# Kernel tuning notes

Measured on AMD Instinct MI355X. Metric: run time of the kernel, lower is better.

Reference implementation:

```python
import jax, jax.numpy as jnp
import numpy as np

B, S, D_IN = 64, 3072, 128
E, H, OUT = 64, 256, 10
K, STRIDE = 3, 3
T_OUT = (S - K) // STRIDE + 1  # 1024


def setup_inputs() -> dict:
    key = jax.random.key(0)
    ks = jax.random.split(key, 8)
    inputs = jax.random.normal(ks[0], (B, S, D_IN), dtype=jnp.float32)
    r = jnp.zeros((B, E, T_OUT), dtype=jnp.float32)
    s = 0.05
    conv_w = jax.random.normal(ks[1], (E, D_IN, K), dtype=jnp.float32) * s
    conv_b = jax.random.normal(ks[2], (E,), dtype=jnp.float32) * s
    w_ih = jax.random.normal(ks[3], (4 * H, E), dtype=jnp.float32) * s
    w_hh = jax.random.normal(ks[4], (4 * H, H), dtype=jnp.float32) * s
    b_ih = jax.random.normal(ks[5], (4 * H,), dtype=jnp.float32) * s
    b_hh = jax.random.normal(ks[6], (4 * H,), dtype=jnp.float32) * s
    lin_w = jax.random.normal(ks[7], (OUT, H), dtype=jnp.float32) * s
    lin_b = jnp.zeros((OUT,), dtype=jnp.float32)
    return {"inputs": inputs, "r": r, "batch_size": B,
            "conv_w": conv_w, "conv_b": conv_b,
            "w_ih": w_ih, "w_hh": w_hh, "b_ih": b_ih, "b_hh": b_hh,
            "lin_w": lin_w, "lin_b": lin_b}


def _forward(inputs, conv_w, conv_b, w_ih, w_hh, b_ih, b_hh, lin_w, lin_b):
    # F.normalize(inputs, dim=2): L2-normalize feature dim (eps=1e-12)
    norm = jnp.linalg.norm(inputs, axis=2, keepdims=True)
    x = inputs / jnp.maximum(norm, 1e-12)
    # permute(0,2,1): [B, D_IN, S], then Conv1d stride 3
    x = jnp.transpose(x, (0, 2, 1))
    emb = jax.lax.conv_general_dilated(
        x, conv_w, window_strides=(STRIDE,), padding='VALID',
        dimension_numbers=('NCH', 'OIH', 'NCH'))
    emb = emb + conv_b[None, :, None]
    act = jax.nn.relu(emb)                      # [B, E, T_OUT]
    xs = jnp.transpose(act, (2, 0, 1))          # [T, B, E] for scan

    def step(carry, x_t):
        h, c = carry
        gates = x_t @ w_ih.T + b_ih + h @ w_hh.T + b_hh  # [B, 4H]
        i_g, f_g, g_g, o_g = jnp.split(gates, 4, axis=1)
        c_new = jax.nn.sigmoid(f_g) * c + jax.nn.sigmoid(i_g) * jnp.tanh(g_g)
        h_new = jax.nn.sigmoid(o_g) * jnp.tanh(c_new)
        return (h_new, c_new), None

    h0 = jnp.zeros((inputs.shape[0], H), dtype=inputs.dtype)
    c0 = jnp.zeros((inputs.shape[0], H), dtype=inputs.dtype)
    (h_last, _), _ = jax.lax.scan(step, (h0, c0), xs)
    return h_last @ lin_w.T + lin_b             # [B, OUT]


def reference(inputs, r, batch_size, conv_w, conv_b, w_ih, w_hh, b_ih, b_hh, lin_w, lin_b):
    # mode='plain': r and batch_size are unused by the math
    return _forward(inputs, conv_w, conv_b, w_ih, w_hh, b_ih, b_hh, lin_w, lin_b)
```

## Files before the change

kernel.cpp:

```cpp
#include <hip/hip_runtime.h>
#include <math.h>

#define B_   64
#define S_   3072
#define DIN  128
#define E_   64
#define H_   256
#define OUT_ 10
#define T_   1024
#define NG   32
#define GB   2
#define NCH  8
#define NLINES 192
#define SLOT 168

#define ACT_BYTES   (B_*E_*T_*4)
#define HBUF_OFF    ACT_BYTES
#define HBUF_BYTES  (NG*2*NLINES*16)
#define HFINAL_OFF  (HBUF_OFF + HBUF_BYTES)
#define HFINAL_BYTES (NG*GB*H_*4)

typedef float f32x4 __attribute__((ext_vector_type(4)));

__device__ __forceinline__ f32x4 coh_load_f32x4(const float* p) {
  f32x4 r;
  asm volatile("global_load_dwordx4 %0, %1, off sc0 sc1\n\ts_waitcnt vmcnt(0)"
               : "=v"(r) : "v"(p) : "memory");
  return r;
}
__device__ __forceinline__ void coh_store_f32x4(float* p, f32x4 v) {
  asm volatile("global_store_dwordx4 %0, %1, off sc0 sc1" :: "v"(p), "v"(v) : "memory");
}

__device__ __forceinline__ float fast_sigmoid(float x) {
  return __builtin_amdgcn_rcpf(1.0f + __expf(-x));
}
__device__ __forceinline__ float fast_tanh(float x) {
  return 2.0f * __builtin_amdgcn_rcpf(1.0f + __expf(-2.0f * x)) - 1.0f;
}

__global__ __launch_bounds__(512, 1) void conv_kernel(
    const float* __restrict__ in,
    const float* __restrict__ cw,
    const float* __restrict__ cb,
    float* __restrict__ actT)
{
  extern __shared__ float xs[];
  float4* xs4 = (float4*)xs;
  const int bid = blockIdx.x;
  const int b  = bid >> 4;
  const int tb = bid & 15;
  const int tid = threadIdx.x;

  const float4* gin = (const float4*)(in + (size_t)b*S_*DIN + (size_t)tb*192*DIN);
  #pragma unroll
  for (int i = 0; i < 12; ++i) {
    int f4 = tid + i*512;
    int r = f4 >> 5, dq = f4 & 31;
    xs4[r*32 + (dq ^ (r & 7))] = gin[f4];
  }
  __syncthreads();

  const int wv = tid >> 6, ln = tid & 63;
  for (int rr = 0; rr < 24; ++rr) {
    int r = wv*24 + rr;
    int u = r*32 + ((ln >> 1) ^ (r & 7));
    float2* p = (float2*)((char*)xs + (size_t)u*16 + (size_t)(ln & 1)*8);
    float2 v = *p;
    float s = v.x*v.x + v.y*v.y;
    #pragma unroll
    for (int off = 32; off >= 1; off >>= 1) s += __shfl_xor(s, off);
    float inv = 1.0f / fmaxf(sqrtf(s), 1e-12f);
    v.x *= inv; v.y *= inv;
    *p = v;
  }
  __syncthreads();

  const int eo = __builtin_amdgcn_readfirstlane(wv);
  float acc[8];
  #pragma unroll
  for (int j = 0; j < 8; ++j) acc[j] = cb[eo*8 + j];

  const int r0 = 3*ln, r1 = 3*ln + 1, r2 = 3*ln + 2;
  #pragma unroll 4
  for (int dq = 0; dq < 32; ++dq) {
    float4 x0 = xs4[r0*32 + (dq ^ (r0 & 7))];
    float4 x1 = xs4[r1*32 + (dq ^ (r1 & 7))];
    float4 x2 = xs4[r2*32 + (dq ^ (r2 & 7))];
    #pragma unroll
    for (int j = 0; j < 8; ++j) {
      const float* wp = cw + (size_t)(eo*8 + j)*(DIN*3) + dq*12;
      acc[j] += x0.x*wp[0] + x1.x*wp[1] + x2.x*wp[2]
              + x0.y*wp[3] + x1.y*wp[4] + x2.y*wp[5]
              + x0.z*wp[6] + x1.z*wp[7] + x2.z*wp[8]
              + x0.w*wp[9] + x1.w*wp[10] + x2.w*wp[11];
    }
  }

  const int tg = tb*64 + ln;
  #pragma unroll
  for (int j = 0; j < 8; ++j) {
    int e = eo*8 + j;
    actT[(size_t)b*E_*T_ + (size_t)e*T_ + tg] = fmaxf(acc[j], 0.0f);
  }
}

__device__ __forceinline__ void kmap(int hidx, int& kh, int& slot) {
  kh = (hidx < 160) ? 0 : 1;
  slot = (hidx < 160) ? hidx : hidx - 160;
}

__global__ __launch_bounds__(512, 1) void lstm_kernel(
    const float* __restrict__ actT,
    const float* __restrict__ w_ih,
    const float* __restrict__ w_hh,
    const float* __restrict__ b_ih,
    const float* __restrict__ b_hh,
    float* hbuf,
    float* hfinal)
{
  __shared__ float sl[2][2][2][SLOT];

  const int bid = blockIdx.x;
  const int g = bid & 31;
  const int q = bid >> 5;
  const int tid = threadIdx.x;
  const int w = tid >> 6;
  const int l = tid & 63;

  const int khalf = l & 1;
  const int m     = (l >> 1) & 3;
  const int o     = l >> 3;
  const int b     = w & 1;
  const int wh    = w >> 1;
  const int hh    = wh*8 + o;
  const int row   = m*256 + 32*q + hh;

  float4 wv[40];
  if (khalf == 0) {
    const float4* ph = (const float4*)(w_hh + (size_t)row*H_);
    #pragma unroll
    for (int i = 0; i < 40; ++i) wv[i] = ph[i];
  } else {
    const float4* ph = (const float4*)(w_hh + (size_t)row*H_) + 40;
    #pragma unroll
    for (int i = 0; i < 24; ++i) wv[i] = ph[i];
    const float4* px = (const float4*)(w_ih + (size_t)row*E_);
    #pragma unroll
    for (int i = 0; i < 16; ++i) wv[24+i] = px[i];
  }
  const float bias = (khalf == 0) ? (b_ih[row] + b_hh[row]) : 0.0f;

  for (int i = tid; i < 2*2*2*SLOT; i += 512) ((float*)sl)[i] = 0.0f;

  const int pq = tid / 24, pw = (tid % 24) / 3, ps = tid % 3;
  const bool is_poll = (tid < 192) && (pq != q);
  const int pb = pw & 1;
  const int phh0 = 32*pq + (pw >> 1)*8 + 3*ps;
  const int pcnt = (ps == 2) ? 2 : 3;

  const bool is_x = (tid >= 384);
  const int xi = tid - 384, xb = (xi >> 6) & 1, xe = xi & 63;
  const float* actp = actT + (size_t)((g*GB + xb)*E_ + xe)*T_;

  const int ss = l / 24;
  const bool is_store = ((l % 24) == 0);
  const int sline = q*24 + w*3 + ss;
  const int shh0 = wh*8 + 3*ss;
  const int scnt = (ss == 2) ? 2 : 3;

  float* hb = hbuf + (size_t)g*(2*NLINES*4);

  __syncthreads();

  float c = 0.0f;
  for (int t = 0; t < T_; ++t) {
    const int p = t & 1;

    float xval = 0.0f;
    if (is_x) xval = actp[t];

    if (t > 0 && is_poll) {
      const float* lp = hb + (size_t)(p*NLINES + tid)*4;
      f32x4 v = coh_load_f32x4(lp);
      while (__float_as_int(v[3]) != t) v = coh_load_f32x4(lp);
      #pragma unroll
      for (int j = 0; j < 3; ++j) {
        if (j < pcnt) {
          int kh, slot; kmap(phh0 + j, kh, slot);
          sl[p][pb][kh][slot] = v[j];
        }
      }
    }
    if (is_x) sl[p][xb][1][96 + xe] = xval;
    __syncthreads();

    float acc = bias;
    {
      const float* hs = &sl[p][b][khalf][0];
      #pragma unroll
      for (int i = 0; i < 40; ++i) {
        float4 h4 = *(const float4*)(hs + i*4);
        acc += wv[i].x*h4.x + wv[i].y*h4.y + wv[i].z*h4.z + wv[i].w*h4.w;
      }
    }

    float ksum = acc + __shfl_xor(acc, 1);
    float x1 = __shfl_xor(ksum, 2);
    float x2 = __shfl_xor(ksum, 4);
    float x3 = __shfl_xor(x1, 4);
    float gi = (m==0)?ksum:(m==1)?x1 :(m==2)?x2 :x3;
    float gf = (m==0)?x1 :(m==1)?ksum:(m==2)?x3 :x2;
    float gg = (m==0)?x2 :(m==1)?x3 :(m==2)?ksum:x1;
    float go = (m==0)?x3 :(m==1)?x2 :(m==2)?x1 :ksum;

    float si = fast_sigmoid(gi);
    float sf = fast_sigmoid(gf);
    float so = fast_sigmoid(go);
    c = sf*c + si*fast_tanh(gg);
    float h = so*fast_tanh(c);

    float v1 = __shfl(h, (l + 8) & 63, 64);
    float v2 = __shfl(h, (l + 16) & 63, 64);
    if (is_store) {
      f32x4 line;
      line[0] = h; line[1] = v1; line[2] = v2;
      line[3] = __int_as_float(t + 1);
      float* dp = hb + (size_t)((((t+1) & 1)*NLINES) + sline)*4;
      coh_store_f32x4(dp, line);
      #pragma unroll
      for (int j = 0; j < 3; ++j) {
        if (j < scnt) {
          int kh, slot; kmap(32*q + shh0 + j, kh, slot);
          sl[p ^ 1][b][kh][slot] = (j == 0) ? h : (j == 1) ? v1 : v2;
        }
      }
      if (t == T_ - 1) {
        #pragma unroll
        for (int j = 0; j < 3; ++j)
          if (j < scnt)
            hfinal[(size_t)g*GB*H_ + (size_t)b*H_ + 32*q + shh0 + j]
                = (j == 0) ? h : (j == 1) ? v1 : v2;
      }
    }
  }
}

__global__ void head_kernel(const float* __restrict__ hfinal,
                            const float* __restrict__ lw,
                            const float* __restrict__ lb,
                            float* __restrict__ out)
{
  int idx = blockIdx.x*blockDim.x + threadIdx.x;
  if (idx >= B_*OUT_) return;
  int b = idx / OUT_, o = idx % OUT_;
  int g = b >> 1, bl = b & 1;
  const float* h = hfinal + (size_t)g*GB*H_ + (size_t)bl*H_;
  const float* wv = lw + (size_t)o*H_;
  float s = lb[o];
  #pragma unroll 8
  for (int k = 0; k < H_; ++k) s += h[k]*wv[k];
  out[idx] = s;
}

extern "C" void kernel_launch(void* const* d_in, const int* in_sizes, int n_in,
                              void* d_out, int out_size, void* d_ws, size_t ws_size,
                              hipStream_t stream) {
  const float* inputs = (const float*)d_in[0];
  const float* conv_w = (const float*)d_in[3];
  const float* conv_b = (const float*)d_in[4];
  const float* w_ih   = (const float*)d_in[5];
  const float* w_hh   = (const float*)d_in[6];
  const float* b_ih   = (const float*)d_in[7];
  const float* b_hh   = (const float*)d_in[8];
  const float* lin_w  = (const float*)d_in[9];
  const float* lin_b  = (const float*)d_in[10];

  float* actT   = (float*)d_ws;
  float* hbuf   = (float*)((char*)d_ws + HBUF_OFF);
  float* hfinal = (float*)((char*)d_ws + HFINAL_OFF);

  hipMemsetAsync(hbuf, 0, HBUF_BYTES, stream);
  hipLaunchKernelGGL(conv_kernel, dim3(B_*16), dim3(512), 192*128*4, stream,
                     inputs, conv_w, conv_b, actT);
  hipLaunchKernelGGL(lstm_kernel, dim3(NG*NCH), dim3(512), 0, stream,
                     actT, w_ih, w_hh, b_ih, b_hh, hbuf, hfinal);
  hipLaunchKernelGGL(head_kernel, dim3(3), dim3(256), 0, stream,
                     hfinal, lin_w, lin_b, (float*)d_out);
}
```

Baseline: 2.118 ms.

## Split LSTM block into compute and polling waves, overlap next-step fetch

The LSTM block now has 4 compute waves that each handle both batch rows, reusing every register-held weight for two dot products. Separate 3 producer waves fetch the next step's inputs and poll for peer h lines into the other LDS buffer while the compute waves work. This leaves one barrier per step instead of a poll-then-barrier-then-compute sequence, hiding global polling latency behind compute. The trade-off is more work per compute wave, which lengthens the critical path per step, plus a more complex h-line layout with 6 lines per wave.

Measured after the change: 3.319 ms. +56.7%, slower.

```diff
diff --git a/kernel.cpp b/kernel.cpp
--- a/kernel.cpp
+++ b/kernel.cpp
@@ -13,6 +13,8 @@
 #define NCH  8
 #define NLINES 192
 #define SLOT 168
+#define CW   4
+#define NTHR 448
 
 #define ACT_BYTES   (B_*E_*T_*4)
 #define HBUF_OFF    ACT_BYTES
@@ -110,7 +112,7 @@
   slot = (hidx < 160) ? hidx : hidx - 160;
 }
 
-__global__ __launch_bounds__(512, 1) void lstm_kernel(
+__global__ __launch_bounds__(NTHR, 1) void lstm_kernel(
     const float* __restrict__ actT,
     const float* __restrict__ w_ih,
     const float* __restrict__ w_hh,
@@ -127,122 +129,152 @@
   const int tid = threadIdx.x;
   const int w = tid >> 6;
   const int l = tid & 63;
+  const bool is_comp = (w < CW);
 
   const int khalf = l & 1;
   const int m     = (l >> 1) & 3;
   const int o     = l >> 3;
-  const int b     = w & 1;
-  const int wh    = w >> 1;
-  const int hh    = wh*8 + o;
+  const int hh    = w*8 + o;
   const int row   = m*256 + 32*q + hh;
 
   float4 wv[40];
-  if (khalf == 0) {
-    const float4* ph = (const float4*)(w_hh + (size_t)row*H_);
-    #pragma unroll
-    for (int i = 0; i < 40; ++i) wv[i] = ph[i];
-  } else {
-    const float4* ph = (const float4*)(w_hh + (size_t)row*H_) + 40;
-    #pragma unroll
-    for (int i = 0; i < 24; ++i) wv[i] = ph[i];
-    const float4* px = (const float4*)(w_ih + (size_t)row*E_);
-    #pragma unroll
-    for (int i = 0; i < 16; ++i) wv[24+i] = px[i];
-  }
-  const float bias = (khalf == 0) ? (b_ih[row] + b_hh[row]) : 0.0f;
-
-  for (int i = tid; i < 2*2*2*SLOT; i += 512) ((float*)sl)[i] = 0.0f;
-
-  const int pq = tid / 24, pw = (tid % 24) / 3, ps = tid % 3;
-  const bool is_poll = (tid < 192) && (pq != q);
-  const int pb = pw & 1;
-  const int phh0 = 32*pq + (pw >> 1)*8 + 3*ps;
-  const int pcnt = (ps == 2) ? 2 : 3;
-
-  const bool is_x = (tid >= 384);
-  const int xi = tid - 384, xb = (xi >> 6) & 1, xe = xi & 63;
+  float bias = 0.0f;
+  if (is_comp) {
+    if (khalf == 0) {
+      const float4* ph = (const float4*)(w_hh + (size_t)row*H_);
+      #pragma unroll
+      for (int i = 0; i < 40; ++i) wv[i] = ph[i];
+      bias = b_ih[row] + b_hh[row];
+    } else {
+      const float4* ph = (const float4*)(w_hh + (size_t)row*H_) + 40;
+      #pragma unroll
+      for (int i = 0; i < 24; ++i) wv[i] = ph[i];
+      const float4* px = (const float4*)(w_ih + (size_t)row*E_);
+      #pragma unroll
+      for (int i = 0; i < 16; ++i) wv[24+i] = px[i];
+    }
+  }
+
+  for (int i = tid; i < 2*2*2*SLOT; i += NTHR) ((float*)sl)[i] = 0.0f;
+
+  const int ss = l >> 3;
+  const bool is_store = is_comp && ((l & 7) == 0) && (ss < 6);
+  const int sline = q*24 + w*6 + ss;
+  const int scnt = (ss == 5) ? 1 : 3;
+
+  const int rl = (w - CW)*64 + l;
+  const bool is_poll = (!is_comp) && (rl < 168);
+  int pline = 0, pq = 0, pw = 0, ps2 = 0;
+  if (is_poll) {
+    int qq = rl / 24;
+    pq = qq + (qq >= q ? 1 : 0);
+    int rest = rl % 24;
+    pw = rest / 6; ps2 = rest % 6;
+    pline = pq*24 + pw*6 + ps2;
+  }
+  const int pcnt = (ps2 == 5) ? 1 : 3;
+  const bool is_x = (!is_comp) && (rl < 128);
+  const int xb = (rl >> 6) & 1, xe = rl & 63;
   const float* actp = actT + (size_t)((g*GB + xb)*E_ + xe)*T_;
 
-  const int ss = l / 24;
-  const bool is_store = ((l % 24) == 0);
-  const int sline = q*24 + w*3 + ss;
-  const int shh0 = wh*8 + 3*ss;
-  const int scnt = (ss == 2) ? 2 : 3;
-
   float* hb = hbuf + (size_t)g*(2*NLINES*4);
 
+  if (is_x) sl[0][xb][1][96 + xe] = actp[0];
   __syncthreads();
 
-  float c = 0.0f;
+  float c0 = 0.0f, c1 = 0.0f;
   for (int t = 0; t < T_; ++t) {
     const int p = t & 1;
 
-    float xval = 0.0f;
-    if (is_x) xval = actp[t];
-
-    if (t > 0 && is_poll) {
-      const float* lp = hb + (size_t)(p*NLINES + tid)*4;
-      f32x4 v = coh_load_f32x4(lp);
-      while (__float_as_int(v[3]) != t) v = coh_load_f32x4(lp);
+    if (is_comp) {
+      float acc0 = bias, acc1 = bias;
+      const float* hs0 = &sl[p][0][khalf][0];
+      const float* hs1 = &sl[p][1][khalf][0];
       #pragma unroll
-      for (int j = 0; j < 3; ++j) {
-        if (j < pcnt) {
-          int kh, slot; kmap(phh0 + j, kh, slot);
-          sl[p][pb][kh][slot] = v[j];
+      for (int i = 0; i < 40; ++i) {
+        float4 a4 = *(const float4*)(hs0 + i*4);
+        float4 b4 = *(const float4*)(hs1 + i*4);
+        acc0 += wv[i].x*a4.x + wv[i].y*a4.y + wv[i].z*a4.z + wv[i].w*a4.w;
+        acc1 += wv[i].x*b4.x + wv[i].y*b4.y + wv[i].z*b4.z + wv[i].w*b4.w;
+      }
+
+      float k0 = acc0 + __shfl_xor(acc0, 1);
+      float k1 = acc1 + __shfl_xor(acc1, 1);
+      float a1 = __shfl_xor(k0, 2), a2 = __shfl_xor(k0, 4), a3 = __shfl_xor(a1, 4);
+      float e1 = __shfl_xor(k1, 2), e2 = __shfl_xor(k1, 4), e3 = __shfl_xor(e1, 4);
+      float gi0 = (m==0)?k0:(m==1)?a1:(m==2)?a2:a3;
+      float gf0 = (m==0)?a1:(m==1)?k0:(m==2)?a3:a2;
+      float gg0 = (m==0)?a2:(m==1)?a3:(m==2)?k0:a1;
+      float go0 = (m==0)?a3:(m==1)?a2:(m==2)?a1:k0;
+      float gi1 = (m==0)?k1:(m==1)?e1:(m==2)?e2:e3;
+      float gf1 = (m==0)?e1:(m==1)?k1:(m==2)?e3:e2;
+      float gg1 = (m==0)?e2:(m==1)?e3:(m==2)?k1:e1;
+      float go1 = (m==0)?e3:(m==1)?e2:(m==2)?e1:k1;
+
+      c0 = fast_sigmoid(gf0)*c0 + fast_sigmoid(gi0)*fast_tanh(gg0);
+      float h0 = fast_sigmoid(go0)*fast_tanh(c0);
+      c1 = fast_sigmoid(gf1)*c1 + fast_sigmoid(gi1)*fast_tanh(gg1);
+      float h1 = fast_sigmoid(go1)*fast_tanh(c1);
+
+      float lv0, lv1, lv2;
+      {
+        int k0i = 3*ss, k1i = 3*ss + 1, k2i = 3*ss + 2;
+        k1i = (k1i > 15) ? 15 : k1i;  k2i = (k2i > 15) ? 15 : k2i;
+        int s0 = 8*((k0i >> 1) & 7), s1 = 8*((k1i >> 1) & 7), s2 = 8*((k2i >> 1) & 7);
+        float t00 = __shfl(h0, s0, 64), t01 = __shfl(h1, s0, 64);
+        float t10 = __shfl(h0, s1, 64), t11 = __shfl(h1, s1, 64);
+        float t20 = __shfl(h0, s2, 64), t21 = __shfl(h1, s2, 64);
+        lv0 = (k0i & 1) ? t01 : t00;
+        lv1 = (k1i & 1) ? t11 : t10;
+        lv2 = (k2i & 1) ? t21 : t20;
+      }
+
+      if (is_store) {
+        f32x4 line;
+        line[0] = lv0; line[1] = lv1; line[2] = lv2;
+        line[3] = __int_as_float(t + 1);
+        float* dp = hb + (size_t)((((t+1) & 1)*NLINES) + sline)*4;
+        coh_store_f32x4(dp, line);
+        #pragma unroll
+        for (int j = 0; j < 3; ++j) {
+          if (j < scnt) {
+            int k = 3*ss + j;
+            int kh, slot; kmap(32*q + w*8 + (k >> 1), kh, slot);
+            sl[p ^ 1][k & 1][kh][slot] = (j == 0) ? lv0 : (j == 1) ? lv1 : lv2;
+          }
+        }
+        if (t == T_ - 1) {
+          #pragma unroll
+          for (int j = 0; j < 3; ++j) {
+            if (j < scnt) {
+              int k = 3*ss + j;
+              hfinal[(size_t)g*GB*H_ + (size_t)(k & 1)*H_ + 32*q + w*8 + (k >> 1)]
+                  = (j == 0) ? lv0 : (j == 1) ? lv1 : lv2;
+            }
+          }
         }
       }
-    }
-    if (is_x) sl[p][xb][1][96 + xe] = xval;
-    __syncthreads();
-
-    float acc = bias;
-    {
-      const float* hs = &sl[p][b][khalf][0];
-      #pragma unroll
-      for (int i = 0; i < 40; ++i) {
-        float4 h4 = *(const float4*)(hs + i*4);
-        acc += wv[i].x*h4.x + wv[i].y*h4.y + wv[i].z*h4.z + wv[i].w*h4.w;
+    } else {
+      if (t < T_ - 1) {
+        float xval = 0.0f;
+        if (is_x) xval = actp[t + 1];
+        if (is_poll) {
+          const float* lp = hb + (size_t)(((t+1) & 1)*NLINES + pline)*4;
+          f32x4 v = coh_load_f32x4(lp);
+          while (__float_as_int(v[3]) != t + 1) v = coh_load_f32x4(lp);
+          #pragma unroll
+          for (int j = 0; j < 3; ++j) {
+            if (j < pcnt) {
+              int k = 3*ps2 + j;
+              int kh, slot; kmap(32*pq + pw*8 + (k >> 1), kh, slot);
+              sl[p ^ 1][k & 1][kh][slot] = v[j];
+            }
+          }
+        }
+        if (is_x) sl[p ^ 1][xb][1][96 + xe] = xval;
       }
     }
-
-    float ksum = acc + __shfl_xor(acc, 1);
-    float x1 = __shfl_xor(ksum, 2);
-    float x2 = __shfl_xor(ksum, 4);
-    float x3 = __shfl_xor(x1, 4);
-    float gi = (m==0)?ksum:(m==1)?x1 :(m==2)?x2 :x3;
-    float gf = (m==0)?x1 :(m==1)?ksum:(m==2)?x3 :x2;
-    float gg = (m==0)?x2 :(m==1)?x3 :(m==2)?ksum:x1;
-    float go = (m==0)?x3 :(m==1)?x2 :(m==2)?x1 :ksum;
-
-    float si = fast_sigmoid(gi);
-    float sf = fast_sigmoid(gf);
-    float so = fast_sigmoid(go);
-    c = sf*c + si*fast_tanh(gg);
-    float h = so*fast_tanh(c);
-
-    float v1 = __shfl(h, (l + 8) & 63, 64);
-    float v2 = __shfl(h, (l + 16) & 63, 64);
-    if (is_store) {
-      f32x4 line;
-      line[0] = h; line[1] = v1; line[2] = v2;
-      line[3] = __int_as_float(t + 1);
-      float* dp = hb + (size_t)((((t+1) & 1)*NLINES) + sline)*4;
-      coh_store_f32x4(dp, line);
-      #pragma unroll
-      for (int j = 0; j < 3; ++j) {
-        if (j < scnt) {
-          int kh, slot; kmap(32*q + shh0 + j, kh, slot);
-          sl[p ^ 1][b][kh][slot] = (j == 0) ? h : (j == 1) ? v1 : v2;
-        }
-      }
-      if (t == T_ - 1) {
-        #pragma unroll
-        for (int j = 0; j < 3; ++j)
-          if (j < scnt)
-            hfinal[(size_t)g*GB*H_ + (size_t)b*H_ + 32*q + shh0 + j]
-                = (j == 0) ? h : (j == 1) ? v1 : v2;
-      }
-    }
+    __syncthreads();
   }
 }
 
@@ -283,7 +315,7 @@
   hipMemsetAsync(hbuf, 0, HBUF_BYTES, stream);
   hipLaunchKernelGGL(conv_kernel, dim3(B_*16), dim3(512), 192*128*4, stream,
                      inputs, conv_w, conv_b, actT);
-  hipLaunchKernelGGL(lstm_kernel, dim3(NG*NCH), dim3(512), 0, stream,
+  hipLaunchKernelGGL(lstm_kernel, dim3(NG*NCH), dim3(NTHR), 0, stream,
                      actT, w_ih, w_hh, b_ih, b_hh, hbuf, hfinal);
   hipLaunchKernelGGL(head_kernel, dim3(3), dim3(256), 0, stream,
                      hfinal, lin_w, lin_b, (float*)d_out);
```

## Redistribute polling across lanes and use lightweight step barrier in LSTM loop

Applied to the files above, without the earlier changes.

Moves the remote-h polling work off threads 0..191 and onto non-store lanes of the first three warps, so no wave polls lines it produces itself. Replaces __syncthreads with a custom barrier that waits only on LDS counters and a scheduling fence, avoiding a full vmcnt drain before each step. It also adds an explicit vmcnt wait after the coherent store. The goal is to shorten the per-timestep critical path of the cross-workgroup recurrent exchange. In exchange it depends on correct memory ordering being kept by hand.

New measurement: 2.201 ms. +3.9%, slower.

```diff
diff --git a/kernel.cpp b/kernel.cpp
--- a/kernel.cpp
+++ b/kernel.cpp
@@ -32,6 +32,12 @@
   asm volatile("global_store_dwordx4 %0, %1, off sc0 sc1" :: "v"(p), "v"(v) : "memory");
 }
 
+__device__ __forceinline__ void step_barrier() {
+  asm volatile("s_waitcnt lgkmcnt(0)" ::: "memory");
+  __builtin_amdgcn_sched_barrier(0);
+  __builtin_amdgcn_s_barrier();
+}
+
 __device__ __forceinline__ float fast_sigmoid(float x) {
   return __builtin_amdgcn_rcpf(1.0f + __expf(-x));
 }
@@ -153,24 +159,35 @@
 
   for (int i = tid; i < 2*2*2*SLOT; i += 512) ((float*)sl)[i] = 0.0f;
 
-  const int pq = tid / 24, pw = (tid % 24) / 3, ps = tid % 3;
-  const bool is_poll = (tid < 192) && (pq != q);
-  const int pb = pw & 1;
-  const int phh0 = 32*pq + (pw >> 1)*8 + 3*ps;
-  const int pcnt = (ps == 2) ? 2 : 3;
-
-  const bool is_x = (tid >= 384);
-  const int xi = tid - 384, xb = (xi >> 6) & 1, xe = xi & 63;
-  const float* actp = actT + (size_t)((g*GB + xb)*E_ + xe)*T_;
-
   const int ss = l / 24;
   const bool is_store = ((l % 24) == 0);
   const int sline = q*24 + w*3 + ss;
   const int shh0 = wh*8 + 3*ss;
   const int scnt = (ss == 2) ? 2 : 3;
 
+  const bool lane_ok = ((l % 24) != 0);
+  const int rank = l - 1 - (l >= 24) - (l >= 48);
+  const int pi = w*61 + rank;
+  const bool is_poll = (w < 3) && lane_ok && (pi < 168);
+  int pline = 0, pb = 0, phh0 = 0, pcnt = 3;
+  if (is_poll) {
+    int qq = pi / 24;
+    int pq = qq + (qq >= q ? 1 : 0);
+    int rest = pi % 24;
+    int pw = rest / 3, ps = rest % 3;
+    pline = pq*24 + pw*3 + ps;
+    pb = pw & 1;
+    phh0 = 32*pq + (pw >> 1)*8 + 3*ps;
+    pcnt = (ps == 2) ? 2 : 3;
+  }
+
+  const bool is_x = (tid >= 384);
+  const int xi = tid - 384, xb = (xi >> 6) & 1, xe = xi & 63;
+  const float* actp = actT + (size_t)((g*GB + xb)*E_ + xe)*T_;
+
   float* hb = hbuf + (size_t)g*(2*NLINES*4);
 
+  if (is_x) sl[0][xb][1][96 + xe] = actp[0];
   __syncthreads();
 
   float c = 0.0f;
@@ -181,7 +198,7 @@
     if (is_x) xval = actp[t];
 
     if (t > 0 && is_poll) {
-      const float* lp = hb + (size_t)(p*NLINES + tid)*4;
+      const float* lp = hb + (size_t)(p*NLINES + pline)*4;
       f32x4 v = coh_load_f32x4(lp);
       while (__float_as_int(v[3]) != t) v = coh_load_f32x4(lp);
       #pragma unroll
@@ -193,7 +210,7 @@
       }
     }
     if (is_x) sl[p][xb][1][96 + xe] = xval;
-    __syncthreads();
+    step_barrier();
 
     float acc = bias;
     {
@@ -242,6 +259,7 @@
             hfinal[(size_t)g*GB*H_ + (size_t)b*H_ + 32*q + shh0 + j]
                 = (j == 0) ? h : (j == 1) ? v1 : v2;
       }
+      asm volatile("s_waitcnt vmcnt(0)" ::: "memory");
     }
   }
 }
```
